# Performance work log

Measured on AMD Instinct MI355X. Metric: run time of the kernel, lower is better.

## Reference

```python
import jax, jax.numpy as jnp
import numpy as np

EPS = 1e-5
B, CIN, COUT, H, W = 32, 512, 512, 56, 56
K = 4            # kernel_num
A = 32           # attention_channel = max(int(512*0.0625), 16)


def setup_inputs() -> dict:
    key = jax.random.key(0)
    ks = jax.random.split(key, 16)
    s = lambda fan: 1.0 / np.sqrt(fan)
    return {
        "x": jax.random.normal(ks[0], (B, CIN, H, W), jnp.float32),
        # attention trunk: global-avgpool -> fc -> bn -> relu
        "fc_w": jax.random.normal(ks[1], (A, CIN), jnp.float32) * s(CIN),
        "abn_g": jnp.ones((A,), jnp.float32),
        "abn_b": jnp.zeros((A,), jnp.float32),
        "abn_m": jax.random.normal(ks[2], (A,), jnp.float32) * 0.1,
        "abn_v": jax.random.uniform(ks[3], (A,), jnp.float32, 0.5, 1.5),
        # channel / filter / kernel attention heads
        "ch_w": jax.random.normal(ks[4], (CIN, A), jnp.float32) * s(A),
        "ch_b": jnp.zeros((CIN,), jnp.float32),
        "fl_w": jax.random.normal(ks[5], (COUT, A), jnp.float32) * s(A),
        "fl_b": jnp.zeros((COUT,), jnp.float32),
        "kn_w": jax.random.normal(ks[6], (K, A), jnp.float32) * s(A),
        "kn_b": jnp.zeros((K,), jnp.float32),
        # base 1x1 conv weight bank [kernel_num, out, in] (1x1 spatial squeezed)
        "weight": jax.random.normal(ks[7], (K, COUT, CIN), jnp.float32) * s(CIN),
        # output BatchNorm2d (eval mode: running stats)
        "bn_g": jnp.ones((COUT,), jnp.float32),
        "bn_b": jnp.zeros((COUT,), jnp.float32),
        "bn_m": jax.random.normal(ks[8], (COUT,), jnp.float32) * 0.1,
        "bn_v": jax.random.uniform(ks[9], (COUT,), jnp.float32, 0.5, 1.5),
    }


def reference(x, fc_w, abn_g, abn_b, abn_m, abn_v,
              ch_w, ch_b, fl_w, fl_b, kn_w, kn_b,
              weight, bn_g, bn_b, bn_m, bn_v):
    # ---- omni-dimensional attention (kernel_size=1 => spatial attn skipped) ----
    pooled = jnp.mean(x, axis=(2, 3))                       # [B, Cin]
    h = pooled @ fc_w.T                                     # [B, A]
    h = (h - abn_m) * (abn_g / jnp.sqrt(abn_v + EPS)) + abn_b
    h = jax.nn.relu(h)
    ch_att = jax.nn.sigmoid(h @ ch_w.T + ch_b)              # [B, Cin]
    fl_att = jax.nn.sigmoid(h @ fl_w.T + fl_b)              # [B, Cout]
    kn_att = jax.nn.softmax(h @ kn_w.T + kn_b, axis=1)      # [B, K] (temperature=1)
    # ---- per-sample aggregated 1x1 kernel + grouped(batch) pointwise conv ----
    agg_w = jnp.einsum('bk,koc->boc', kn_att, weight)       # [B, Cout, Cin]
    xm = x * ch_att[:, :, None, None]                       # channel attention
    y = jnp.einsum('bchw,boc->bohw', xm, agg_w)             # batched 1x1 conv
    y = y * fl_att[:, :, None, None]                        # filter attention
    # ---- BatchNorm2d (inference) ----
    inv = bn_g / jnp.sqrt(bn_v + EPS)
    y = (y - bn_m[None, :, None, None]) * inv[None, :, None, None] + bn_b[None, :, None, None]
    return y
```

## Files before the change

### kernel.cpp

```cpp
#include <hip/hip_runtime.h>
#include <math.h>

#define BATCH 32
#define CIN   512
#define COUT  512
#define HW    3136
#define KNUM  4
#define ADIM  32
#define EPS   1e-5f

static constexpr size_t XT_OFF     = 0;
static constexpr size_t WF_OFF     = 102760448;
static constexpr size_t POOLED_OFF = 119537664;
static constexpr size_t H_OFF      = 119603200;
static constexpr size_t CH_OFF     = 119607296;
static constexpr size_t FLINV_OFF  = 119672832;
static constexpr size_t KN_OFF     = 119738368;
static constexpr size_t BETA_OFF   = 119738880;

typedef __attribute__((ext_vector_type(8))) short short8;
typedef __attribute__((ext_vector_type(4))) float float4v;

typedef const unsigned int __attribute__((address_space(1)))* gas_ptr;
typedef unsigned int __attribute__((address_space(3)))* lds_ptr;

__device__ __forceinline__ unsigned short f2bf(float f) {
  unsigned int u = __float_as_uint(f);
  u += 0x7FFFu + ((u >> 16) & 1u);
  return (unsigned short)(u >> 16);
}

__global__ void zero_f32(float* __restrict__ p, int n) {
  int i = blockIdx.x * blockDim.x + threadIdx.x;
  if (i < n) p[i] = 0.f;
}

__global__ __launch_bounds__(256) void transpose_pool(
    const float* __restrict__ x, unsigned short* __restrict__ xT,
    float* __restrict__ pooled) {
  __shared__ unsigned short T[64 * 68];
  const int pb = blockIdx.x * 64;
  const int cb = blockIdx.y * 64;
  const int b  = blockIdx.z;
  const int t  = threadIdx.x;
  const int mp = t & 15;
  const int mc = t >> 4;
  const int c0 = cb + mc * 4;
  const int p0 = pb + mp * 4;

  const float* xp = x + (size_t)(b * CIN + c0) * HW + p0;
  float a[4][4];
  #pragma unroll
  for (int r = 0; r < 4; ++r) {
    float4 v = *(const float4*)(xp + (size_t)r * HW);
    a[r][0] = v.x; a[r][1] = v.y; a[r][2] = v.z; a[r][3] = v.w;
    float s = v.x + v.y + v.z + v.w;
    #pragma unroll
    for (int off = 8; off > 0; off >>= 1) s += __shfl_down(s, off, 16);
    if (mp == 0) atomicAdd(&pooled[b * CIN + c0 + r], s);
  }
  #pragma unroll
  for (int j = 0; j < 4; ++j) {
    ushort4 w;
    w.x = f2bf(a[0][j]); w.y = f2bf(a[1][j]);
    w.z = f2bf(a[2][j]); w.w = f2bf(a[3][j]);
    *(ushort4*)&T[(mp * 4 + j) * 68 + mc * 4] = w;
  }
  __syncthreads();
  const int pr = t >> 2, cp = t & 3;
  const int base = pr * 68 + cp * 16;
  uint2 r0 = *(uint2*)&T[base + 0];
  uint2 r1 = *(uint2*)&T[base + 4];
  uint2 r2 = *(uint2*)&T[base + 8];
  uint2 r3 = *(uint2*)&T[base + 12];
  unsigned short* dst = xT + (size_t)(b * HW + pb + pr) * CIN + cb + cp * 16;
  *(uint4*)(dst)     = make_uint4(r0.x, r0.y, r1.x, r1.y);
  *(uint4*)(dst + 8) = make_uint4(r2.x, r2.y, r3.x, r3.y);
}

__global__ __launch_bounds__(256) void attn_h_kn(
    const float* __restrict__ pooled, const float* __restrict__ fc_w,
    const float* __restrict__ abn_g, const float* __restrict__ abn_b,
    const float* __restrict__ abn_m, const float* __restrict__ abn_v,
    const float* __restrict__ kn_w, const float* __restrict__ kn_b,
    float* __restrict__ h_out, float* __restrict__ kn_out) {
  __shared__ float hs[ADIM];
  const int b = blockIdx.x, t = threadIdx.x;
  const int a = t >> 3, part = t & 7;
  const float* pr = pooled + b * CIN;
  const float* fr = fc_w + a * CIN;
  float s = 0.f;
  const int cb = part * 64;
  #pragma unroll 8
  for (int c = 0; c < 64; ++c) s += pr[cb + c] * fr[cb + c];
  #pragma unroll
  for (int off = 4; off > 0; off >>= 1) s += __shfl_down(s, off, 8);
  if (part == 0) {
    s *= (1.0f / (float)HW);
    float vv = (s - abn_m[a]) * (abn_g[a] * rsqrtf(abn_v[a] + EPS)) + abn_b[a];
    vv = fmaxf(vv, 0.f);
    hs[a] = vv;
    h_out[b * ADIM + a] = vv;
  }
  __syncthreads();
  if (t == 0) {
    float lg[KNUM]; float mx = -1e30f;
    for (int k = 0; k < KNUM; ++k) {
      float acc = kn_b[k];
      for (int aa = 0; aa < ADIM; ++aa) acc += hs[aa] * kn_w[k * ADIM + aa];
      lg[k] = acc; mx = fmaxf(mx, acc);
    }
    float ssum = 0.f;
    for (int k = 0; k < KNUM; ++k) { lg[k] = expf(lg[k] - mx); ssum += lg[k]; }
    for (int k = 0; k < KNUM; ++k) kn_out[b * KNUM + k] = lg[k] / ssum;
  }
}

__global__ void beta_kernel(const float* __restrict__ bn_g, const float* __restrict__ bn_b,
                            const float* __restrict__ bn_m, const float* __restrict__ bn_v,
                            float* __restrict__ beta) {
  int o = blockIdx.x * 256 + threadIdx.x;
  if (o < COUT) {
    float inv = bn_g[o] * rsqrtf(bn_v[o] + EPS);
    beta[o] = bn_b[o] - bn_m[o] * inv;
  }
}

__global__ __launch_bounds__(128) void attn_heads(
    const float* __restrict__ h, const float* __restrict__ ch_w, const float* __restrict__ ch_b,
    const float* __restrict__ fl_w, const float* __restrict__ fl_b,
    const float* __restrict__ bn_g, const float* __restrict__ bn_v,
    float* __restrict__ ch_out, float* __restrict__ flinv_out) {
  __shared__ float hs[ADIM];
  const int ck = blockIdx.x, b = blockIdx.y, t = threadIdx.x;
  if (t < ADIM) hs[t] = h[b * ADIM + t];
  __syncthreads();
  if (ck < 4) {
    int c = ck * 128 + t;
    const float* wr = ch_w + c * ADIM;
    float acc = ch_b[c];
    #pragma unroll
    for (int aa = 0; aa < ADIM; ++aa) acc += hs[aa] * wr[aa];
    ch_out[b * CIN + c] = 1.f / (1.f + expf(-acc));
  } else {
    int o = (ck - 4) * 128 + t;
    const float* wr = fl_w + o * ADIM;
    float acc = fl_b[o];
    #pragma unroll
    for (int aa = 0; aa < ADIM; ++aa) acc += hs[aa] * wr[aa];
    float sig = 1.f / (1.f + expf(-acc));
    flinv_out[b * COUT + o] = sig * (bn_g[o] * rsqrtf(bn_v[o] + EPS));
  }
}

__global__ __launch_bounds__(256) void build_wf(
    const float* __restrict__ weight, const float* __restrict__ kn,
    const float* __restrict__ ch, const float* __restrict__ flinv,
    unsigned short* __restrict__ Wf) {
  const int och = blockIdx.x, b = blockIdx.y, t = threadIdx.x;
  const int o0 = och * 16;
  const float k0 = kn[b * KNUM + 0], k1 = kn[b * KNUM + 1];
  const float k2 = kn[b * KNUM + 2], k3 = kn[b * KNUM + 3];
  #pragma unroll
  for (int i = 0; i < 8; ++i) {
    int cell = i * 1024 + t * 4;
    int ol = cell >> 9, c = cell & 511;
    int o = o0 + ol;
    float fi = flinv[b * COUT + o];
    const float* wp = weight + (size_t)o * CIN + c;
    float4 w0 = *(const float4*)(wp);
    float4 w1 = *(const float4*)(wp + 1 * CIN * COUT);
    float4 w2 = *(const float4*)(wp + 2 * CIN * COUT);
    float4 w3 = *(const float4*)(wp + 3 * CIN * COUT);
    float4 cv = *(const float4*)(ch + b * CIN + c);
    ushort4 r;
    r.x = f2bf((k0 * w0.x + k1 * w1.x + k2 * w2.x + k3 * w3.x) * cv.x * fi);
    r.y = f2bf((k0 * w0.y + k1 * w1.y + k2 * w2.y + k3 * w3.y) * cv.y * fi);
    r.z = f2bf((k0 * w0.z + k1 * w1.z + k2 * w2.z + k3 * w3.z) * cv.z * fi);
    r.w = f2bf((k0 * w0.w + k1 * w1.w + k2 * w2.w + k3 * w3.w) * cv.w * fi);
    *(ushort4*)(Wf + (size_t)(b * COUT + o) * CIN + c) = r;
  }
}

__global__ __launch_bounds__(256) void gemm_kernel(
    const unsigned short* __restrict__ xT, const unsigned short* __restrict__ Wf,
    const float* __restrict__ beta, float* __restrict__ y) {
  __shared__ unsigned short lA[128 * 32];
  __shared__ unsigned short lB[128 * 32];
  const int pt = blockIdx.x, ot = blockIdx.y, b = blockIdx.z;
  const int o0 = ot * 128, p0 = pt * 128;
  const int t = threadIdx.x;
  const int wave = t >> 6, lane = t & 63;
  const int wm = wave & 1, wn = wave >> 1;

  const int lrow = lane >> 2;
  const int lcol = (lane & 3) * 8;
  const int r0 = (wave * 2 + 0) * 16 + lrow;
  const int r1 = (wave * 2 + 1) * 16 + lrow;

  const unsigned short* Ab = Wf + (size_t)b * COUT * CIN;
  const unsigned short* Bb = xT + (size_t)b * HW * CIN;
  const unsigned short* agp0 = Ab + (size_t)(o0 + r0) * CIN + lcol;
  const unsigned short* agp1 = Ab + (size_t)(o0 + r1) * CIN + lcol;
  int bp0 = p0 + r0; if (bp0 > HW - 1) bp0 = HW - 1;
  int bp1 = p0 + r1; if (bp1 > HW - 1) bp1 = HW - 1;
  const unsigned short* bgp0 = Bb + (size_t)bp0 * CIN + lcol;
  const unsigned short* bgp1 = Bb + (size_t)bp1 * CIN + lcol;

  unsigned short* lA0 = &lA[(wave * 2 + 0) * 512];
  unsigned short* lA1 = &lA[(wave * 2 + 1) * 512];
  unsigned short* lB0 = &lB[(wave * 2 + 0) * 512];
  unsigned short* lB1 = &lB[(wave * 2 + 1) * 512];

  float4v acc[4][4];
  #pragma unroll
  for (int i = 0; i < 4; ++i)
    #pragma unroll
    for (int j = 0; j < 4; ++j)
      #pragma unroll
      for (int r = 0; r < 4; ++r) acc[i][j][r] = 0.f;

  const int arow = lane & 15;
  const int kofs = (lane >> 4) * 8;

  for (int kt = 0; kt < CIN / 32; ++kt) {
    const int c0 = kt * 32;
    __syncthreads();
    __builtin_amdgcn_global_load_lds((gas_ptr)(const void*)(agp0 + c0), (lds_ptr)(void*)lA0, 16, 0, 0);
    __builtin_amdgcn_global_load_lds((gas_ptr)(const void*)(agp1 + c0), (lds_ptr)(void*)lA1, 16, 0, 0);
    __builtin_amdgcn_global_load_lds((gas_ptr)(const void*)(bgp0 + c0), (lds_ptr)(void*)lB0, 16, 0, 0);
    __builtin_amdgcn_global_load_lds((gas_ptr)(const void*)(bgp1 + c0), (lds_ptr)(void*)lB1, 16, 0, 0);
    __syncthreads();

    short8 af[4], bfr[4];
    #pragma unroll
    for (int i = 0; i < 4; ++i)
      af[i] = *(const short8*)&lA[(wm * 64 + i * 16 + arow) * 32 + kofs];
    #pragma unroll
    for (int j = 0; j < 4; ++j)
      bfr[j] = *(const short8*)&lB[(wn * 64 + j * 16 + arow) * 32 + kofs];
    #pragma unroll
    for (int i = 0; i < 4; ++i)
      #pragma unroll
      for (int j = 0; j < 4; ++j)
        acc[i][j] = __builtin_amdgcn_mfma_f32_16x16x32_bf16(af[i], bfr[j], acc[i][j], 0, 0, 0);
  }

  const int rowq = (lane >> 4) * 4;
  const int coln = lane & 15;
  #pragma unroll
  for (int i = 0; i < 4; ++i) {
    const int obase = o0 + wm * 64 + i * 16 + rowq;
    float bet[4];
    #pragma unroll
    for (int r = 0; r < 4; ++r) bet[r] = beta[obase + r];
    #pragma unroll
    for (int j = 0; j < 4; ++j) {
      const int p = p0 + wn * 64 + j * 16 + coln;
      if (p < HW) {
        #pragma unroll
        for (int r = 0; r < 4; ++r)
          y[(size_t)(b * COUT + obase + r) * HW + p] = acc[i][j][r] + bet[r];
      }
    }
  }
}

extern "C" void kernel_launch(void* const* d_in, const int* in_sizes, int n_in,
                              void* d_out, int out_size, void* d_ws, size_t ws_size,
                              hipStream_t stream) {
  (void)in_sizes; (void)n_in; (void)out_size; (void)ws_size;
  const float* x     = (const float*)d_in[0];
  const float* fc_w  = (const float*)d_in[1];
  const float* abn_g = (const float*)d_in[2];
  const float* abn_b = (const float*)d_in[3];
  const float* abn_m = (const float*)d_in[4];
  const float* abn_v = (const float*)d_in[5];
  const float* ch_w  = (const float*)d_in[6];
  const float* ch_b  = (const float*)d_in[7];
  const float* fl_w  = (const float*)d_in[8];
  const float* fl_b  = (const float*)d_in[9];
  const float* kn_w  = (const float*)d_in[10];
  const float* kn_b  = (const float*)d_in[11];
  const float* weight= (const float*)d_in[12];
  const float* bn_g  = (const float*)d_in[13];
  const float* bn_b  = (const float*)d_in[14];
  const float* bn_m  = (const float*)d_in[15];
  const float* bn_v  = (const float*)d_in[16];
  float* out = (float*)d_out;

  char* ws = (char*)d_ws;
  unsigned short* xT   = (unsigned short*)(ws + XT_OFF);
  unsigned short* Wf   = (unsigned short*)(ws + WF_OFF);
  float* pooled = (float*)(ws + POOLED_OFF);
  float* h      = (float*)(ws + H_OFF);
  float* ch     = (float*)(ws + CH_OFF);
  float* flinv  = (float*)(ws + FLINV_OFF);
  float* kn     = (float*)(ws + KN_OFF);
  float* beta   = (float*)(ws + BETA_OFF);

  zero_f32<<<64, 256, 0, stream>>>(pooled, BATCH * CIN);
  transpose_pool<<<dim3(HW / 64, CIN / 64, BATCH), 256, 0, stream>>>(x, xT, pooled);
  attn_h_kn<<<BATCH, 256, 0, stream>>>(pooled, fc_w, abn_g, abn_b, abn_m, abn_v,
                                       kn_w, kn_b, h, kn);
  beta_kernel<<<2, 256, 0, stream>>>(bn_g, bn_b, bn_m, bn_v, beta);
  attn_heads<<<dim3(8, BATCH), 128, 0, stream>>>(h, ch_w, ch_b, fl_w, fl_b, bn_g, bn_v,
                                                 ch, flinv);
  build_wf<<<dim3(32, BATCH), 256, 0, stream>>>(weight, kn, ch, flinv, Wf);
  gemm_kernel<<<dim3(25, 4, BATCH), 256, 0, stream>>>(xT, Wf, beta, out);
}
```

Measured before the change: 501.8 us.

## Double-buffer GEMM LDS tiles, XOR-swizzle LDS layout, and remap blocks per XCD

The GEMM kernel now keeps two LDS buffers, so it prefetches the next K-slice via global_load_lds while issuing MFMAs on the current one, with one barrier per iteration instead of two. LDS column slots are XOR-swizzled by row on both the store and read sides to reduce bank conflicts on the short8 fragment loads. The 3D grid is flattened to 1D and remapped so that blocks landing on the same XCD share batch and pixel tiles, improving L2 reuse. LDS use doubles, which may lower occupancy, and the overlap depends on the compiler not inserting a full vmcnt wait before the LDS reads.

After: 522.8 us. 1.04x slower.

```diff
diff --git a/kernel.cpp b/kernel.cpp
--- a/kernel.cpp
+++ b/kernel.cpp
@@ -185,32 +185,34 @@
 __global__ __launch_bounds__(256) void gemm_kernel(
     const unsigned short* __restrict__ xT, const unsigned short* __restrict__ Wf,
     const float* __restrict__ beta, float* __restrict__ y) {
-  __shared__ unsigned short lA[128 * 32];
-  __shared__ unsigned short lB[128 * 32];
-  const int pt = blockIdx.x, ot = blockIdx.y, b = blockIdx.z;
+  __shared__ unsigned short lA[2][128 * 32];
+  __shared__ unsigned short lB[2][128 * 32];
+
+  const int lin = blockIdx.x;
+  const int xcd = lin & 7;
+  const int jj  = lin >> 3;
+  const int ot  = jj & 3;
+  const int pair = xcd * 100 + (jj >> 2);
+  const int b  = pair / 25;
+  const int pt = pair % 25;
   const int o0 = ot * 128, p0 = pt * 128;
   const int t = threadIdx.x;
   const int wave = t >> 6, lane = t & 63;
   const int wm = wave & 1, wn = wave >> 1;
 
   const int lrow = lane >> 2;
-  const int lcol = (lane & 3) * 8;
+  const int csw  = (((lane & 3) ^ ((lrow >> 1) & 3))) * 8;
   const int r0 = (wave * 2 + 0) * 16 + lrow;
   const int r1 = (wave * 2 + 1) * 16 + lrow;
 
   const unsigned short* Ab = Wf + (size_t)b * COUT * CIN;
   const unsigned short* Bb = xT + (size_t)b * HW * CIN;
-  const unsigned short* agp0 = Ab + (size_t)(o0 + r0) * CIN + lcol;
-  const unsigned short* agp1 = Ab + (size_t)(o0 + r1) * CIN + lcol;
+  const unsigned short* agp0 = Ab + (size_t)(o0 + r0) * CIN + csw;
+  const unsigned short* agp1 = Ab + (size_t)(o0 + r1) * CIN + csw;
   int bp0 = p0 + r0; if (bp0 > HW - 1) bp0 = HW - 1;
   int bp1 = p0 + r1; if (bp1 > HW - 1) bp1 = HW - 1;
-  const unsigned short* bgp0 = Bb + (size_t)bp0 * CIN + lcol;
-  const unsigned short* bgp1 = Bb + (size_t)bp1 * CIN + lcol;
-
-  unsigned short* lA0 = &lA[(wave * 2 + 0) * 512];
-  unsigned short* lA1 = &lA[(wave * 2 + 1) * 512];
-  unsigned short* lB0 = &lB[(wave * 2 + 0) * 512];
-  unsigned short* lB1 = &lB[(wave * 2 + 1) * 512];
+  const unsigned short* bgp0 = Bb + (size_t)bp0 * CIN + csw;
+  const unsigned short* bgp1 = Bb + (size_t)bp1 * CIN + csw;
 
   float4v acc[4][4];
   #pragma unroll
@@ -221,29 +223,49 @@
       for (int r = 0; r < 4; ++r) acc[i][j][r] = 0.f;
 
   const int arow = lane & 15;
-  const int kofs = (lane >> 4) * 8;
-
+  const int kgrp = lane >> 4;
+  const int ksw  = (kgrp ^ ((arow >> 1) & 3)) * 8;
+
+  {
+    unsigned short* dA0 = &lA[0][(wave * 2 + 0) * 512];
+    unsigned short* dA1 = &lA[0][(wave * 2 + 1) * 512];
+    unsigned short* dB0 = &lB[0][(wave * 2 + 0) * 512];
+    unsigned short* dB1 = &lB[0][(wave * 2 + 1) * 512];
+    __builtin_amdgcn_global_load_lds((gas_ptr)(const void*)(agp0), (lds_ptr)(void*)dA0, 16, 0, 0);
+    __builtin_amdgcn_global_load_lds((gas_ptr)(const void*)(agp1), (lds_ptr)(void*)dA1, 16, 0, 0);
+    __builtin_amdgcn_global_load_lds((gas_ptr)(const void*)(bgp0), (lds_ptr)(void*)dB0, 16, 0, 0);
+    __builtin_amdgcn_global_load_lds((gas_ptr)(const void*)(bgp1), (lds_ptr)(void*)dB1, 16, 0, 0);
+  }
+
+  int cur = 0;
   for (int kt = 0; kt < CIN / 32; ++kt) {
-    const int c0 = kt * 32;
     __syncthreads();
-    __builtin_amdgcn_global_load_lds((gas_ptr)(const void*)(agp0 + c0), (lds_ptr)(void*)lA0, 16, 0, 0);
-    __builtin_amdgcn_global_load_lds((gas_ptr)(const void*)(agp1 + c0), (lds_ptr)(void*)lA1, 16, 0, 0);
-    __builtin_amdgcn_global_load_lds((gas_ptr)(const void*)(bgp0 + c0), (lds_ptr)(void*)lB0, 16, 0, 0);
-    __builtin_amdgcn_global_load_lds((gas_ptr)(const void*)(bgp1 + c0), (lds_ptr)(void*)lB1, 16, 0, 0);
-    __syncthreads();
+    if (kt + 1 < CIN / 32) {
+      const int c1 = (kt + 1) * 32;
+      const int nb = cur ^ 1;
+      unsigned short* dA0 = &lA[nb][(wave * 2 + 0) * 512];
+      unsigned short* dA1 = &lA[nb][(wave * 2 + 1) * 512];
+      unsigned short* dB0 = &lB[nb][(wave * 2 + 0) * 512];
+      unsigned short* dB1 = &lB[nb][(wave * 2 + 1) * 512];
+      __builtin_amdgcn_global_load_lds((gas_ptr)(const void*)(agp0 + c1), (lds_ptr)(void*)dA0, 16, 0, 0);
+      __builtin_amdgcn_global_load_lds((gas_ptr)(const void*)(agp1 + c1), (lds_ptr)(void*)dA1, 16, 0, 0);
+      __builtin_amdgcn_global_load_lds((gas_ptr)(const void*)(bgp0 + c1), (lds_ptr)(void*)dB0, 16, 0, 0);
+      __builtin_amdgcn_global_load_lds((gas_ptr)(const void*)(bgp1 + c1), (lds_ptr)(void*)dB1, 16, 0, 0);
+    }
 
     short8 af[4], bfr[4];
     #pragma unroll
     for (int i = 0; i < 4; ++i)
-      af[i] = *(const short8*)&lA[(wm * 64 + i * 16 + arow) * 32 + kofs];
+      af[i] = *(const short8*)&lA[cur][(wm * 64 + i * 16 + arow) * 32 + ksw];
     #pragma unroll
     for (int j = 0; j < 4; ++j)
-      bfr[j] = *(const short8*)&lB[(wn * 64 + j * 16 + arow) * 32 + kofs];
+      bfr[j] = *(const short8*)&lB[cur][(wn * 64 + j * 16 + arow) * 32 + ksw];
     #pragma unroll
     for (int i = 0; i < 4; ++i)
       #pragma unroll
       for (int j = 0; j < 4; ++j)
         acc[i][j] = __builtin_amdgcn_mfma_f32_16x16x32_bf16(af[i], bfr[j], acc[i][j], 0, 0, 0);
+    cur ^= 1;
   }
 
   const int rowq = (lane >> 4) * 4;
@@ -307,5 +329,5 @@
   attn_heads<<<dim3(8, BATCH), 128, 0, stream>>>(h, ch_w, ch_b, fl_w, fl_b, bn_g, bn_v,
                                                  ch, flinv);
   build_wf<<<dim3(32, BATCH), 256, 0, stream>>>(weight, kn, ch, flinv, Wf);
-  gemm_kernel<<<dim3(25, 4, BATCH), 256, 0, stream>>>(xT, Wf, beta, out);
-}
+  gemm_kernel<<<dim3(3200), 256, 0, stream>>>(xT, Wf, beta, out);
+}
```
